# Kernel optimization log

Measured on AMD Instinct MI355X. Metric: run time of the kernel, lower is better.

Reference implementation:

```python
import jax, jax.numpy as jnp
import numpy as np

N = 100000
E = 800000
IN_DIM = 128
H = 4
D = 32
HD = H * D  # 128
EPS = 1e-5
NEG_SLOPE = 0.2


def setup_inputs() -> dict:
    key = jax.random.key(0)
    ks = jax.random.split(key, 12)
    feat = jax.random.normal(ks[0], (N, IN_DIM), dtype=jnp.float32)
    src = jax.random.randint(ks[1], (E,), 0, N)
    dst = jax.random.randint(ks[2], (E,), 0, N)
    s = 1.0 / np.sqrt(IN_DIM)
    W_src = jax.random.uniform(ks[3], (HD, IN_DIM), jnp.float32, -s, s)
    b_src = jax.random.uniform(ks[4], (HD,), jnp.float32, -s, s)
    attn_l = jax.random.normal(ks[5], (1, H, D), dtype=jnp.float32) * np.sqrt(2.0 / (H * D + 1)) * np.sqrt(2.0)
    attn_r = jax.random.normal(ks[6], (1, H, D), dtype=jnp.float32) * np.sqrt(2.0 / (H * D + 1)) * np.sqrt(2.0)
    W_skip = jax.random.uniform(ks[7], (HD, IN_DIM), jnp.float32, -s, s)
    b_skip = jax.random.uniform(ks[8], (HD,), jnp.float32, -s, s)
    sg = 1.0 / np.sqrt(3 * HD)
    W_gate = jax.random.uniform(ks[9], (1, 3 * HD), jnp.float32, -sg, sg)
    b_gate = jax.random.uniform(ks[10], (1,), jnp.float32, -sg, sg)
    ln_g = jnp.ones((HD,), jnp.float32)
    ln_b = jnp.zeros((HD,), jnp.float32)
    prelu_a = jnp.full((1,), 0.25, jnp.float32)
    return {"feat": feat, "src": src, "dst": dst, "W_src": W_src, "b_src": b_src,
            "attn_l": attn_l, "attn_r": attn_r, "W_skip": W_skip, "b_skip": b_skip,
            "W_gate": W_gate, "b_gate": b_gate, "ln_g": ln_g, "ln_b": ln_b,
            "prelu_a": prelu_a}


def reference(feat, src, dst, W_src, b_src, attn_l, attn_r, W_skip, b_skip,
              W_gate, b_gate, ln_g, ln_b, prelu_a):
    # node projection -> [N, H, D]
    feat_src = (feat @ W_src.T + b_src).reshape(N, H, D)
    el = jnp.sum(feat_src * attn_l, axis=-1)  # [N, H]
    er = jnp.sum(feat_src * attn_r, axis=-1)  # [N, H]
    # per-edge logits with leaky relu
    e = el[src] + er[dst]                      # [E, H]
    e = jnp.where(e >= 0, e, NEG_SLOPE * e)
    # edge softmax over incoming edges of each dst node
    emax = jax.ops.segment_max(e, dst, num_segments=N)   # [N, H]
    ex = jnp.exp(e - emax[dst])                          # [E, H]
    esum = jax.ops.segment_sum(ex, dst, num_segments=N)  # [N, H]
    a = ex / esum[dst]                                   # [E, H]
    # weighted aggregation: sum_e a_e * ft[src_e]
    m = feat_src[src] * a[:, :, None]                    # [E, H, D]
    rst = jax.ops.segment_sum(m, dst, num_segments=N).reshape(N, HD)
    # gated skip connection
    skip = feat @ W_skip.T + b_skip                      # [N, HD]
    g_in = jnp.concatenate([rst, skip, rst - skip], axis=-1)
    gate = jax.nn.sigmoid(g_in @ W_gate.T + b_gate)      # [N, 1]
    rst = gate * rst + (1.0 - gate) * skip
    # layer norm
    mu = jnp.mean(rst, axis=-1, keepdims=True)
    var = jnp.var(rst, axis=-1, keepdims=True)
    y = (rst - mu) / jnp.sqrt(var + EPS) * ln_g + ln_b
    # PReLU (single shared alpha)
    return jnp.where(y >= 0, y, prelu_a[0] * y)
```

## Files before the change

### kernel.cpp

```cpp
#include <hip/hip_runtime.h>

typedef __attribute__((ext_vector_type(8))) short short8;
typedef __attribute__((ext_vector_type(4))) float v4f;

__device__ __forceinline__ ushort f2bf(float x) {
    unsigned u = __float_as_uint(x);
    u = u + 0x7fffu + ((u >> 16) & 1u);
    return (ushort)(u >> 16);
}
__device__ __forceinline__ float bflo(unsigned u) { return __uint_as_float(u << 16); }
__device__ __forceinline__ float bfhi(unsigned u) { return __uint_as_float(u & 0xffff0000u); }

#define CPAD 16
#define SLOT 64
#define GGRID 512

__global__ __launch_bounds__(256) void k_prepedge(
    const float* __restrict__ Wsrc, const float* __restrict__ Wskip,
    ushort* __restrict__ Wb, const int* __restrict__ src,
    const int* __restrict__ dst, int* __restrict__ counts_p,
    int* __restrict__ padcsr, int E_, int neb)
{
    int b = blockIdx.x;
    if (b < neb) {
        int e = (b * 256 + threadIdx.x) * 2;
        if (e + 1 < E_) {
            int2 d2 = *(const int2*)(dst + e);
            int2 s2 = *(const int2*)(src + e);
            int r0 = atomicAdd(&counts_p[(size_t)d2.x * CPAD], 1);
            int r1 = atomicAdd(&counts_p[(size_t)d2.y * CPAD], 1);
            if (r0 < SLOT) padcsr[(size_t)d2.x * SLOT + r0] = s2.x;
            if (r1 < SLOT) padcsr[(size_t)d2.y * SLOT + r1] = s2.y;
        } else if (e < E_) {
            int d = dst[e];
            int r = atomicAdd(&counts_p[(size_t)d * CPAD], 1);
            if (r < SLOT) padcsr[(size_t)d * SLOT + r] = src[e];
        }
    } else {
        int i = (b - neb) * 256 + threadIdx.x;
        float v = (i < 16384) ? Wsrc[i] : Wskip[i - 16384];
        Wb[i] = f2bf(v);
    }
}

__global__ __launch_bounds__(256, 2) void k_gemm(
    const float* __restrict__ feat, const ushort* __restrict__ Wb,
    const float* __restrict__ bsrc, const float* __restrict__ bskip,
    const float* __restrict__ attn_l, const float* __restrict__ attn_r,
    ushort* __restrict__ feat_src, ushort* __restrict__ skip_bf,
    float* __restrict__ el, float* __restrict__ er, int n)
{
    __shared__ float sA[8192];
    const int tid = threadIdx.x;
    const int wave = tid >> 6, lane = tid & 63;
    const int quad = lane >> 4, l16 = lane & 15;
    const int n0 = wave * 64;
    const int ntile = (n + 31) >> 5;

    const ushort* bp = Wb + (size_t)(n0 + l16) * 128 + quad * 8;
    short8 bb[4][4];
    #pragma unroll
    for (int nt = 0; nt < 4; ++nt)
        #pragma unroll
        for (int k = 0; k < 4; ++k) {
            bb[nt][k] = *(const short8*)(bp + nt * 2048 + k * 32);
            asm volatile("" : "+v"(bb[nt][k]));
        }

    float4 bias[4], al[4], ar[4];
    #pragma unroll
    for (int nt = 0; nt < 4; ++nt) {
        int cb = n0 + nt * 16 + quad * 4;
        bias[nt] = (n0 < 128) ? *(const float4*)(bsrc + cb)
                              : *(const float4*)(bskip + (cb - 128));
        al[nt] = *(const float4*)(attn_l + ((cb) & 127));
        ar[nt] = *(const float4*)(attn_r + ((cb) & 127));
    }

    const int trow = tid >> 5;
    const int scb  = ((tid & 31) * 16) ^ ((trow & 7) << 4);
    const char* gbase = (const char*)feat;

    auto stage = [&](int tt, int buf) {
        #pragma unroll
        for (int i = 0; i < 4; ++i) {
            int grow = tt * 32 + i * 8 + trow;
            if (grow > n - 1) grow = n - 1;
            const void* g = gbase + (size_t)grow * 512 + scb;
            float* lp = sA + buf * 4096 + i * 1024 + wave * 256;
            __builtin_amdgcn_global_load_lds(
                (const __attribute__((address_space(1))) void*)g,
                (__attribute__((address_space(3))) void*)lp, 16, 0, 0);
        }
    };

    int t = blockIdx.x;
    if (t >= ntile) return;
    stage(t, 0);
    int p = 0;
    bool first = true;

    for (; t < ntile; t += GGRID) {
        int tn = t + GGRID;
        bool pre = (tn < ntile);
        if (pre) stage(tn, p ^ 1);
        if (!pre)       asm volatile("s_waitcnt vmcnt(0)" ::: "memory");
        else if (first) asm volatile("s_waitcnt vmcnt(4)" ::: "memory");
        else            asm volatile("s_waitcnt vmcnt(8)" ::: "memory");
        first = false;
        __builtin_amdgcn_s_barrier();
        __builtin_amdgcn_sched_barrier(0);

        const int row0 = t * 32;
        v4f acc[2][4] = {};
        const char* sAB = (const char*)sA + p * 16384;
        const int sw = (l16 & 7) << 4;
        #pragma unroll
        for (int k = 0; k < 4; ++k) {
            int c = quad * 32 + k * 128;
            float4 f0 = *(const float4*)(sAB + l16 * 512 + ((c     ) ^ sw));
            float4 f1 = *(const float4*)(sAB + l16 * 512 + ((c + 16) ^ sw));
            float4 g0 = *(const float4*)(sAB + (l16 + 16) * 512 + ((c     ) ^ sw));
            float4 g1 = *(const float4*)(sAB + (l16 + 16) * 512 + ((c + 16) ^ sw));
            short8 a0, a1;
            a0[0] = (short)f2bf(f0.x); a0[1] = (short)f2bf(f0.y);
            a0[2] = (short)f2bf(f0.z); a0[3] = (short)f2bf(f0.w);
            a0[4] = (short)f2bf(f1.x); a0[5] = (short)f2bf(f1.y);
            a0[6] = (short)f2bf(f1.z); a0[7] = (short)f2bf(f1.w);
            a1[0] = (short)f2bf(g0.x); a1[1] = (short)f2bf(g0.y);
            a1[2] = (short)f2bf(g0.z); a1[3] = (short)f2bf(g0.w);
            a1[4] = (short)f2bf(g1.x); a1[5] = (short)f2bf(g1.y);
            a1[6] = (short)f2bf(g1.z); a1[7] = (short)f2bf(g1.w);
            #pragma unroll
            for (int nt = 0; nt < 4; ++nt) {
                acc[0][nt] = __builtin_amdgcn_mfma_f32_16x16x32_bf16(
                    bb[nt][k], a0, acc[0][nt], 0, 0, 0);
                acc[1][nt] = __builtin_amdgcn_mfma_f32_16x16x32_bf16(
                    bb[nt][k], a1, acc[1][nt], 0, 0, 0);
            }
        }

        #pragma unroll
        for (int nt = 0; nt < 4; ++nt) {
            #pragma unroll
            for (int mt = 0; mt < 2; ++mt) {
                acc[mt][nt][0] += bias[nt].x;
                acc[mt][nt][1] += bias[nt].y;
                acc[mt][nt][2] += bias[nt].z;
                acc[mt][nt][3] += bias[nt].w;
            }
        }

        #pragma unroll
        for (int mt = 0; mt < 2; ++mt) {
            int row = row0 + mt * 16 + l16;
            if (row < n) {
                #pragma unroll
                for (int nt = 0; nt < 4; ++nt) {
                    int cb = n0 + nt * 16 + quad * 4;
                    unsigned lo = (unsigned)f2bf(acc[mt][nt][0]) |
                                  ((unsigned)f2bf(acc[mt][nt][1]) << 16);
                    unsigned hi = (unsigned)f2bf(acc[mt][nt][2]) |
                                  ((unsigned)f2bf(acc[mt][nt][3]) << 16);
                    uint2 pv = make_uint2(lo, hi);
                    if (n0 < 128) *(uint2*)(feat_src + (size_t)row * 128 + cb) = pv;
                    else          *(uint2*)(skip_bf  + (size_t)row * 128 + (cb - 128)) = pv;
                }
            }
        }

        if (wave < 2) {
            const int hb = n0 >> 5;
            #pragma unroll
            for (int mt = 0; mt < 2; ++mt) {
                float pl0 = 0.f, pl1 = 0.f, pr0 = 0.f, pr1 = 0.f;
                #pragma unroll
                for (int i = 0; i < 4; ++i) {
                    float a0v = acc[mt][0][i], a1v = acc[mt][1][i];
                    float a2v = acc[mt][2][i], a3v = acc[mt][3][i];
                    const float* pal0 = (const float*)&al[0]; const float* pal1 = (const float*)&al[1];
                    const float* pal2 = (const float*)&al[2]; const float* pal3 = (const float*)&al[3];
                    const float* par0 = (const float*)&ar[0]; const float* par1 = (const float*)&ar[1];
                    const float* par2 = (const float*)&ar[2]; const float* par3 = (const float*)&ar[3];
                    pl0 = fmaf(a0v, pal0[i], fmaf(a1v, pal1[i], pl0));
                    pl1 = fmaf(a2v, pal2[i], fmaf(a3v, pal3[i], pl1));
                    pr0 = fmaf(a0v, par0[i], fmaf(a1v, par1[i], pr0));
                    pr1 = fmaf(a2v, par2[i], fmaf(a3v, par3[i], pr1));
                }
                pl0 += __shfl_xor(pl0, 16); pl0 += __shfl_xor(pl0, 32);
                pl1 += __shfl_xor(pl1, 16); pl1 += __shfl_xor(pl1, 32);
                pr0 += __shfl_xor(pr0, 16); pr0 += __shfl_xor(pr0, 32);
                pr1 += __shfl_xor(pr1, 16); pr1 += __shfl_xor(pr1, 32);
                int row = row0 + mt * 16 + l16;
                if (lane < 16 && row < n) {
                    *(float2*)(el + (size_t)row * 4 + hb) = make_float2(pl0, pl1);
                    *(float2*)(er + (size_t)row * 4 + hb) = make_float2(pr0, pr1);
                }
            }
        }

        __builtin_amdgcn_s_barrier();
        p ^= 1;
    }
}

__global__ __launch_bounds__(256) void k3_fused(
    const int* __restrict__ counts_p, const int* __restrict__ padcsr,
    const float* __restrict__ el, const float* __restrict__ er,
    const ushort* __restrict__ feat_src, const ushort* __restrict__ skip_bf,
    const float* __restrict__ Wg, const float* __restrict__ bg,
    const float* __restrict__ lng, const float* __restrict__ lnb,
    const float* __restrict__ pa, float* __restrict__ out, int n)
{
    int node = blockIdx.x * 8 + (threadIdx.x >> 5);
    if (node >= n) return;
    int l32 = threadIdx.x & 31;
    int j = l32 * 4;
    int h = l32 >> 3;

    int cnt = counts_p[(size_t)node * CPAD];
    if (cnt > SLOT) cnt = SLOT;
    int beg = node * SLOT, end = beg + cnt;
    float er_h = er[(size_t)node * 4 + h];
    const ushort* fbase = feat_src + j;

    float ac0 = 0.f, ac1 = 0.f, ac2 = 0.f, ac3 = 0.f;
    float bc0 = 0.f, bc1 = 0.f, bc2 = 0.f, bc3 = 0.f;
    float wsA = 0.f, wsB = 0.f;

    for (int p0 = beg; p0 < end; p0 += 32) {
        int pv = p0 + l32;
        int sv = padcsr[pv < end ? pv : end - 1];
        int cb = end - p0; if (cb > 32) cb = 32;
        for (int i = 0; i < cb; i += 4) {
            int s0 = __shfl(sv, i, 32),     s1 = __shfl(sv, i + 1, 32);
            int s2 = __shfl(sv, i + 2, 32), s3 = __shfl(sv, i + 3, 32);
            float e0 = el[(size_t)s0 * 4 + h], e1 = el[(size_t)s1 * 4 + h];
            float e2 = el[(size_t)s2 * 4 + h], e3 = el[(size_t)s3 * 4 + h];
            uint2 u0 = *(const uint2*)(fbase + (size_t)s0 * 128);
            uint2 u1 = *(const uint2*)(fbase + (size_t)s1 * 128);
            uint2 u2 = *(const uint2*)(fbase + (size_t)s2 * 128);
            uint2 u3 = *(const uint2*)(fbase + (size_t)s3 * 128);
            float t0 = e0 + er_h, t1 = e1 + er_h, t2 = e2 + er_h, t3 = e3 + er_h;
            float w0 = __expf(t0 >= 0.f ? t0 : 0.2f * t0);
            float w1 = (i + 1 < cb) ? __expf(t1 >= 0.f ? t1 : 0.2f * t1) : 0.f;
            float w2 = (i + 2 < cb) ? __expf(t2 >= 0.f ? t2 : 0.2f * t2) : 0.f;
            float w3 = (i + 3 < cb) ? __expf(t3 >= 0.f ? t3 : 0.2f * t3) : 0.f;
            wsA += w0 + w2; wsB += w1 + w3;
            ac0 = fmaf(w0, bflo(u0.x), fmaf(w2, bflo(u2.x), ac0));
            ac1 = fmaf(w0, bfhi(u0.x), fmaf(w2, bfhi(u2.x), ac1));
            ac2 = fmaf(w0, bflo(u0.y), fmaf(w2, bflo(u2.y), ac2));
            ac3 = fmaf(w0, bfhi(u0.y), fmaf(w2, bfhi(u2.y), ac3));
            bc0 = fmaf(w1, bflo(u1.x), fmaf(w3, bflo(u3.x), bc0));
            bc1 = fmaf(w1, bfhi(u1.x), fmaf(w3, bfhi(u3.x), bc1));
            bc2 = fmaf(w1, bflo(u1.y), fmaf(w3, bflo(u3.y), bc2));
            bc3 = fmaf(w1, bfhi(u1.y), fmaf(w3, bfhi(u3.y), bc3));
        }
    }
    float wsum = wsA + wsB;
    float inv = (wsum > 0.f) ? 1.f / wsum : 0.f;
    float r0 = (ac0 + bc0) * inv, r1 = (ac1 + bc1) * inv;
    float r2 = (ac2 + bc2) * inv, r3 = (ac3 + bc3) * inv;

    uint2 su = *(const uint2*)(skip_bf + (size_t)node * 128 + j);
    float s0 = bflo(su.x), s1 = bfhi(su.x), s2 = bflo(su.y), s3 = bfhi(su.y);

    float4 wg0 = *(const float4*)(Wg + j);
    float4 wg1 = *(const float4*)(Wg + 128 + j);
    float4 wg2 = *(const float4*)(Wg + 256 + j);
    float g = r0 * wg0.x + s0 * wg1.x + (r0 - s0) * wg2.x
            + r1 * wg0.y + s1 * wg1.y + (r1 - s1) * wg2.y
            + r2 * wg0.z + s2 * wg1.z + (r2 - s2) * wg2.z
            + r3 * wg0.w + s3 * wg1.w + (r3 - s3) * wg2.w;
    #pragma unroll
    for (int m = 1; m < 32; m <<= 1) g += __shfl_xor(g, m, 32);
    float gate = 1.f / (1.f + __expf(-(g + bg[0])));

    float x0 = gate * r0 + (1.f - gate) * s0;
    float x1 = gate * r1 + (1.f - gate) * s1;
    float x2 = gate * r2 + (1.f - gate) * s2;
    float x3 = gate * r3 + (1.f - gate) * s3;

    float sm = (x0 + x1) + (x2 + x3);
    float sq = (x0 * x0 + x1 * x1) + (x2 * x2 + x3 * x3);
    #pragma unroll
    for (int m = 1; m < 32; m <<= 1) {
        sm += __shfl_xor(sm, m, 32);
        sq += __shfl_xor(sq, m, 32);
    }
    float mu = sm * (1.f / 128.f);
    float var = sq * (1.f / 128.f) - mu * mu;
    float rs = rsqrtf(var + 1e-5f);
    float alpha = pa[0];
    float4 lg = *(const float4*)(lng + j);
    float4 lb = *(const float4*)(lnb + j);
    float y0 = (x0 - mu) * rs * lg.x + lb.x;
    float y1 = (x1 - mu) * rs * lg.y + lb.y;
    float y2 = (x2 - mu) * rs * lg.z + lb.z;
    float y3 = (x3 - mu) * rs * lg.w + lb.w;
    y0 = y0 >= 0.f ? y0 : alpha * y0;
    y1 = y1 >= 0.f ? y1 : alpha * y1;
    y2 = y2 >= 0.f ? y2 : alpha * y2;
    y3 = y3 >= 0.f ? y3 : alpha * y3;
    *(float4*)(out + (size_t)node * 128 + j) = make_float4(y0, y1, y2, y3);
}

extern "C" void kernel_launch(void* const* d_in, const int* in_sizes, int n_in,
                              void* d_out, int out_size, void* d_ws, size_t ws_size,
                              hipStream_t stream)
{
    const float* feat   = (const float*)d_in[0];
    const int*   src    = (const int*)d_in[1];
    const int*   dst    = (const int*)d_in[2];
    const float* Wsrc   = (const float*)d_in[3];
    const float* bsrc   = (const float*)d_in[4];
    const float* attn_l = (const float*)d_in[5];
    const float* attn_r = (const float*)d_in[6];
    const float* Wskip  = (const float*)d_in[7];
    const float* bskip  = (const float*)d_in[8];
    const float* Wg     = (const float*)d_in[9];
    const float* bg     = (const float*)d_in[10];
    const float* lng    = (const float*)d_in[11];
    const float* lnb    = (const float*)d_in[12];
    const float* pa     = (const float*)d_in[13];

    const int n = in_sizes[0] / 128;
    const int E = in_sizes[1];
    float* out = (float*)d_out;

    float*  el       = (float*)d_ws;
    float*  er       = el + (size_t)n * 4;
    ushort* feat_src = (ushort*)(er + (size_t)n * 4);
    ushort* skip_bf  = feat_src + (size_t)n * 128;
    ushort* Wb       = skip_bf + (size_t)n * 128;
    int*    counts_p = (int*)(Wb + 32768);
    int*    padcsr   = counts_p + (size_t)n * CPAD;

    hipMemsetAsync(counts_p, 0, (size_t)n * CPAD * sizeof(int), stream);

    int neb = (E / 2 + 255) / 256;
    k_prepedge<<<neb + 128, 256, 0, stream>>>(
        Wsrc, Wskip, Wb, src, dst, counts_p, padcsr, E, neb);

    k_gemm<<<GGRID, 256, 0, stream>>>(
        feat, Wb, bsrc, bskip, attn_l, attn_r, feat_src, skip_bf, el, er, n);

    k3_fused<<<(n + 7) / 8, 256, 0, stream>>>(
        counts_p, padcsr, el, er, feat_src, skip_bf, Wg, bg, lng, lnb, pa, out, n);
}
```

Baseline: 244.1 us.

## Partition edge scatter by destination slice and convert weights inside GEMM

```diff
diff --git a/kernel.cpp b/kernel.cpp
--- a/kernel.cpp
+++ b/kernel.cpp
@@ -14,37 +14,55 @@
 #define CPAD 16
 #define SLOT 64
 #define GGRID 512
-
-__global__ __launch_bounds__(256) void k_prepedge(
-    const float* __restrict__ Wsrc, const float* __restrict__ Wskip,
-    ushort* __restrict__ Wb, const int* __restrict__ src,
-    const int* __restrict__ dst, int* __restrict__ counts_p,
-    int* __restrict__ padcsr, int E_, int neb)
+#define CHSZ 4096
+
+__global__ __launch_bounds__(256) void k_edges(
+    const int* __restrict__ src, const int* __restrict__ dst,
+    int* __restrict__ counts_p, int* __restrict__ padcsr,
+    int E_, int ns8, int n)
 {
-    int b = blockIdx.x;
-    if (b < neb) {
-        int e = (b * 256 + threadIdx.x) * 2;
-        if (e + 1 < E_) {
-            int2 d2 = *(const int2*)(dst + e);
-            int2 s2 = *(const int2*)(src + e);
-            int r0 = atomicAdd(&counts_p[(size_t)d2.x * CPAD], 1);
-            int r1 = atomicAdd(&counts_p[(size_t)d2.y * CPAD], 1);
-            if (r0 < SLOT) padcsr[(size_t)d2.x * SLOT + r0] = s2.x;
-            if (r1 < SLOT) padcsr[(size_t)d2.y * SLOT + r1] = s2.y;
-        } else if (e < E_) {
-            int d = dst[e];
-            int r = atomicAdd(&counts_p[(size_t)d * CPAD], 1);
-            if (r < SLOT) padcsr[(size_t)d * SLOT + r] = src[e];
-        }
-    } else {
-        int i = (b - neb) * 256 + threadIdx.x;
-        float v = (i < 16384) ? Wsrc[i] : Wskip[i - 16384];
-        Wb[i] = f2bf(v);
+    const int slice = blockIdx.x & 7;
+    const int chunk = blockIdx.x >> 3;
+    const int lo = slice * ns8;
+    int hi = lo + ns8; if (hi > n) hi = n;
+    const unsigned span = (unsigned)(hi - lo);
+
+    int cend = (chunk + 1) * CHSZ; if (cend > E_) cend = E_;
+    for (int off = chunk * CHSZ + threadIdx.x * 4; off < cend; off += 1024) {
+        if (off + 4 <= cend) {
+            int4 d4 = *(const int4*)(dst + off);
+            int4 s4 = *(const int4*)(src + off);
+            if ((unsigned)(d4.x - lo) < span) {
+                int r = atomicAdd(&counts_p[(size_t)d4.x * CPAD], 1);
+                if (r < SLOT) padcsr[(size_t)d4.x * SLOT + r] = s4.x;
+            }
+            if ((unsigned)(d4.y - lo) < span) {
+                int r = atomicAdd(&counts_p[(size_t)d4.y * CPAD], 1);
+                if (r < SLOT) padcsr[(size_t)d4.y * SLOT + r] = s4.y;
+            }
+            if ((unsigned)(d4.z - lo) < span) {
+                int r = atomicAdd(&counts_p[(size_t)d4.z * CPAD], 1);
+                if (r < SLOT) padcsr[(size_t)d4.z * SLOT + r] = s4.z;
+            }
+            if ((unsigned)(d4.w - lo) < span) {
+                int r = atomicAdd(&counts_p[(size_t)d4.w * CPAD], 1);
+                if (r < SLOT) padcsr[(size_t)d4.w * SLOT + r] = s4.w;
+            }
+        } else {
+            for (int q = off; q < cend; ++q) {
+                int d = dst[q];
+                if ((unsigned)(d - lo) < span) {
+                    int r = atomicAdd(&counts_p[(size_t)d * CPAD], 1);
+                    if (r < SLOT) padcsr[(size_t)d * SLOT + r] = src[q];
+                }
+            }
+        }
     }
 }
 
 __global__ __launch_bounds__(256, 2) void k_gemm(
-    const float* __restrict__ feat, const ushort* __restrict__ Wb,
+    const float* __restrict__ feat, const float* __restrict__ Wsrc,
+    const float* __restrict__ Wskip,
     const float* __restrict__ bsrc, const float* __restrict__ bskip,
     const float* __restrict__ attn_l, const float* __restrict__ attn_r,
     ushort* __restrict__ feat_src, ushort* __restrict__ skip_bf,
@@ -57,15 +75,25 @@
     const int n0 = wave * 64;
     const int ntile = (n + 31) >> 5;
 
-    const ushort* bp = Wb + (size_t)(n0 + l16) * 128 + quad * 8;
     short8 bb[4][4];
     #pragma unroll
-    for (int nt = 0; nt < 4; ++nt)
+    for (int nt = 0; nt < 4; ++nt) {
+        int r = n0 + l16 + nt * 16;
+        const float* wr = (r < 128) ? (Wsrc + (size_t)r * 128)
+                                    : (Wskip + (size_t)(r - 128) * 128);
         #pragma unroll
         for (int k = 0; k < 4; ++k) {
-            bb[nt][k] = *(const short8*)(bp + nt * 2048 + k * 32);
+            float4 w0 = *(const float4*)(wr + quad * 8 + k * 32);
+            float4 w1 = *(const float4*)(wr + quad * 8 + k * 32 + 4);
+            short8 v;
+            v[0] = (short)f2bf(w0.x); v[1] = (short)f2bf(w0.y);
+            v[2] = (short)f2bf(w0.z); v[3] = (short)f2bf(w0.w);
+            v[4] = (short)f2bf(w1.x); v[5] = (short)f2bf(w1.y);
+            v[6] = (short)f2bf(w1.z); v[7] = (short)f2bf(w1.w);
+            bb[nt][k] = v;
             asm volatile("" : "+v"(bb[nt][k]));
         }
+    }
 
     float4 bias[4], al[4], ar[4];
     #pragma unroll
@@ -73,8 +101,8 @@
         int cb = n0 + nt * 16 + quad * 4;
         bias[nt] = (n0 < 128) ? *(const float4*)(bsrc + cb)
                               : *(const float4*)(bskip + (cb - 128));
-        al[nt] = *(const float4*)(attn_l + ((cb) & 127));
-        ar[nt] = *(const float4*)(attn_r + ((cb) & 127));
+        al[nt] = *(const float4*)(attn_l + (cb & 127));
+        ar[nt] = *(const float4*)(attn_r + (cb & 127));
     }
 
     const int trow = tid >> 5;
@@ -332,18 +360,19 @@
     float*  er       = el + (size_t)n * 4;
     ushort* feat_src = (ushort*)(er + (size_t)n * 4);
     ushort* skip_bf  = feat_src + (size_t)n * 128;
-    ushort* Wb       = skip_bf + (size_t)n * 128;
-    int*    counts_p = (int*)(Wb + 32768);
+    int*    counts_p = (int*)(skip_bf + (size_t)n * 128);
     int*    padcsr   = counts_p + (size_t)n * CPAD;
 
     hipMemsetAsync(counts_p, 0, (size_t)n * CPAD * sizeof(int), stream);
 
-    int neb = (E / 2 + 255) / 256;
-    k_prepedge<<<neb + 128, 256, 0, stream>>>(
-        Wsrc, Wskip, Wb, src, dst, counts_p, padcsr, E, neb);
+    int ns8 = (n + 7) / 8;
+    int nchunk = (E + CHSZ - 1) / CHSZ;
+    k_edges<<<nchunk * 8, 256, 0, stream>>>(
+        src, dst, counts_p, padcsr, E, ns8, n);
 
     k_gemm<<<GGRID, 256, 0, stream>>>(
-        feat, Wb, bsrc, bskip, attn_l, attn_r, feat_src, skip_bf, el, er, n);
+        feat, Wsrc, Wskip, bsrc, bskip, attn_l, attn_r,
+        feat_src, skip_bf, el, er, n);
 
     k3_fused<<<(n + 7) / 8, 256, 0, stream>>>(
         counts_p, padcsr, el, er, feat_src, skip_bf, Wg, bg, lng, lnb, pa, out, n);
```

Measured after the change: 237.0 us. -2.9%, faster.
